# Kernel tuning notes

Measured on AMD Instinct MI355X. Metric: run time of the kernel, lower is better.

## Reference

```python
import jax, jax.numpy as jnp
import numpy as np

N_NODES = 50000
N_EDGES = 800000
D = 128


def setup_inputs() -> dict:
    key = jax.random.key(0)
    ks = jax.random.split(key, 8)
    s = 1.0 / np.sqrt(D)
    return {
        "x": jax.random.normal(ks[0], (N_NODES, D), dtype=jnp.float32),
        "edge_index": jax.random.randint(ks[1], (2, N_EDGES), 0, N_NODES, dtype=jnp.int32),
        "W0l": jax.random.normal(ks[2], (D, D), dtype=jnp.float32) * s,
        "b0l": jnp.zeros((D,), dtype=jnp.float32),
        "W0r": jax.random.normal(ks[3], (D, D), dtype=jnp.float32) * s,
        "W1l": jax.random.normal(ks[4], (D, D), dtype=jnp.float32) * s,
        "b1l": jnp.zeros((D,), dtype=jnp.float32),
        "W1r": jax.random.normal(ks[5], (D, D), dtype=jnp.float32) * s,
    }


def reference(x, edge_index, W0l, b0l, W0r, W1l, b1l, W1r):
    # Encoder(conv='sage', num_layers=2), eval mode (dropout = identity).
    src = edge_index[0]  # x_j gathered from source nodes
    dst = edge_index[1]  # aggregated at target nodes
    # in-degree for mean aggregation; isolated nodes get 0 aggregate (PyG mean)
    deg = jax.ops.segment_sum(jnp.ones_like(dst, dtype=x.dtype), dst, num_segments=N_NODES)
    inv_deg = jnp.where(deg > 0, 1.0 / jnp.maximum(deg, 1.0), 0.0)[:, None]

    def sage(h, Wl, bl, Wr):
        m = h @ Wl + bl                                        # lin_l
        agg = jax.ops.segment_sum(m[src], dst, num_segments=N_NODES) * inv_deg  # mean aggr
        return agg + h @ Wr                                    # + lin_r skip

    h = jax.nn.relu(sage(x, W0l, b0l, W0r))   # layer 0 + relu
    return sage(h, W1l, b1l, W1r)             # final layer
```

## Files before the change

kernel.cpp:

```cpp
#include <hip/hip_runtime.h>

#define N_NODES 50000
#define N_EDGES 800000
#define D 128
#define NBLK ((N_NODES + 255) / 256)
#define EPB 4096
#define CAP 8192

typedef __bf16 bf16x8 __attribute__((ext_vector_type(8)));
typedef short s16x8 __attribute__((ext_vector_type(8)));
typedef float f32x4 __attribute__((ext_vector_type(4)));
typedef unsigned short u16;
typedef unsigned int u32;
typedef u32 u32x2 __attribute__((ext_vector_type(2)));

__device__ inline u16 f32_to_bf16(float f) {
    u32 u = __builtin_bit_cast(u32, f);
    u += 0x7fffu + ((u >> 16) & 1u);
    return (u16)(u >> 16);
}
__device__ inline float bf16_lo(u32 v) { return __builtin_bit_cast(float, v << 16); }
__device__ inline float bf16_hi(u32 v) { return __builtin_bit_cast(float, v & 0xffff0000u); }

__device__ inline f32x4 mfma16(s16x8 a, s16x8 b, f32x4 c) {
    return __builtin_amdgcn_mfma_f32_16x16x32_bf16(
        __builtin_bit_cast(bf16x8, a), __builtin_bit_cast(bf16x8, b), c, 0, 0, 0);
}

#define CAST_BLOCKS ((N_NODES * 16) / 256)

__global__ __launch_bounds__(256) void prep_cast(
    const float* __restrict__ x, u16* __restrict__ xb,
    const float* __restrict__ W0l, const float* __restrict__ W0r,
    const float* __restrict__ W1l, const float* __restrict__ W1r,
    u16* __restrict__ Wp) {
    int b = blockIdx.x;
    if (b < CAST_BLOCKS) {
        int gid = b * 256 + threadIdx.x;
        const float* p = x + (size_t)gid * 8;
        f32x4 a = *(const f32x4*)p;
        f32x4 c = *(const f32x4*)(p + 4);
        u16 o[8];
#pragma unroll
        for (int j = 0; j < 4; j++) { o[j] = f32_to_bf16(a[j]); o[4 + j] = f32_to_bf16(c[j]); }
        *(s16x8*)(xb + (size_t)gid * 8) = *(const s16x8*)o;
    } else {
        int gid = (b - CAST_BLOCKS) * 256 + threadIdx.x;
        int wsel = gid >> 11;
        int rem  = gid & 2047;
        int ct   = rem >> 8;
        int ks   = (rem >> 6) & 3;
        int lane = rem & 63;
        const float* W = (wsel == 0) ? W0l : (wsel == 1) ? W0r : (wsel == 2) ? W1l : W1r;
        int n  = ct * 16 + (lane & 15);
        int k0 = ks * 32 + (lane >> 4) * 8;
        u16 o[8];
#pragma unroll
        for (int j = 0; j < 8; j++) o[j] = f32_to_bf16(W[(k0 + j) * D + n]);
        u16* dst = Wp + wsel * 16384 + (size_t)((ct * 4 + ks) * 64 + lane) * 8;
        *(s16x8*)dst = *(const s16x8*)o;
    }
}

__global__ __launch_bounds__(256) void stage_kernel(const int* __restrict__ src,
                                                    const int* __restrict__ dst,
                                                    int* __restrict__ ccount,
                                                    u32* __restrict__ staged) {
    __shared__ int hist[NBLK];
    __shared__ int base[NBLK];
    int t = threadIdx.x, b = blockIdx.x;
    int bb = b * EPB;
    if (t < NBLK) hist[t] = 0;
    __syncthreads();
    u32 pk[16]; int cb[16];
#pragma unroll
    for (int i = 0; i < 16; i++) {
        int e = bb + i * 256 + t;
        if (e < N_EDGES) {
            int sv = src[e], dv = dst[e];
            pk[i] = (u32)sv | ((u32)(dv & 255) << 16);
            cb[i] = dv >> 8;
            atomicAdd(&hist[cb[i]], 1);
        } else cb[i] = -1;
    }
    __syncthreads();
    if (t < NBLK) {
        int c = hist[t];
        if (c > 0) {
            int old = atomicAdd(&ccount[t], c);
            if (old > CAP - c) old = CAP - c;
            base[t] = t * CAP + old;
        }
        hist[t] = 0;
    }
    __syncthreads();
#pragma unroll
    for (int i = 0; i < 16; i++) {
        if (cb[i] >= 0) {
            int slot = atomicAdd(&hist[cb[i]], 1);
            staged[base[cb[i]] + slot] = pk[i];
        }
    }
}

__global__ __launch_bounds__(256) void fine_kernel(const int* __restrict__ ccount,
                                                   const u32* __restrict__ staged,
                                                   u16* __restrict__ eidx,
                                                   int* __restrict__ rowptr,
                                                   float* __restrict__ inv) {
    __shared__ u32 sdata[CAP];
    __shared__ int hist[256];
    __shared__ int cursor[256];
    __shared__ int sc[256];
    __shared__ int wsum[4];
    int t = threadIdx.x, cb = blockIdx.x;
    int lane = t & 63, wave = t >> 6;

    int cc = (t < NBLK) ? ccount[t] : 0;
    int cv = cc > CAP ? CAP : cc;
    int s = cv;
#pragma unroll
    for (int off = 1; off < 64; off <<= 1) {
        int u = __shfl_up(s, off, 64);
        if (lane >= off) s += u;
    }
    if (lane == 63) wsum[wave] = s;
    hist[t] = 0;
    __syncthreads();
    int wadd = 0;
#pragma unroll
    for (int w = 0; w < 4; w++) if (w < wave) wadd += wsum[w];
    sc[t] = s - cv + wadd;
    __syncthreads();
    int gbase = sc[cb];
    int c = ccount[cb];
    if (c > CAP) c = CAP;

    for (int i = t; i < c; i += 256) {
        u32 v = staged[cb * CAP + i];
        sdata[i] = v;
        atomicAdd(&hist[(v >> 16) & 255], 1);
    }
    __syncthreads();
    int d = hist[t];
    s = d;
#pragma unroll
    for (int off = 1; off < 64; off <<= 1) {
        int u = __shfl_up(s, off, 64);
        if (lane >= off) s += u;
    }
    if (lane == 63) wsum[wave] = s;
    __syncthreads();
    wadd = 0;
#pragma unroll
    for (int w = 0; w < 4; w++) if (w < wave) wadd += wsum[w];
    int excl = gbase + s - d + wadd;
    int node = cb * 256 + t;
    if (node < N_NODES) {
        rowptr[node] = excl;
        inv[node] = d > 0 ? 1.0f / (float)d : 0.0f;
    }
    cursor[t] = excl;
    if (cb == 0 && t == 0) rowptr[N_NODES] = N_EDGES;
    __syncthreads();
    for (int i = t; i < c; i += 256) {
        u32 v = sdata[i];
        int pos = atomicAdd(&cursor[(v >> 16) & 255], 1);
        eidx[pos] = (u16)(v & 0xffffu);
    }
}

__global__ __launch_bounds__(256) void agg_mean(const u16* __restrict__ h,
                                                const int* __restrict__ rowptr,
                                                const u16* __restrict__ eidx,
                                                const float* __restrict__ inv,
                                                u16* __restrict__ mean) {
    int wave = threadIdx.x >> 6, lane = threadIdx.x & 63;
    int node = blockIdx.x * 4 + wave;
    if (node >= N_NODES) return;
    int half = lane >> 5;
    int hl = lane & 31;
    int start = rowptr[node], end = rowptr[node + 1];

    float a0 = 0.f, a1 = 0.f, a2 = 0.f, a3 = 0.f;
    int e = start + half;
    for (; e + 6 < end; e += 8) {
        int s0 = eidx[e], s1 = eidx[e + 2], s2 = eidx[e + 4], s3 = eidx[e + 6];
        u32x2 v0 = *(const u32x2*)(h + (size_t)s0 * D + hl * 4);
        u32x2 v1 = *(const u32x2*)(h + (size_t)s1 * D + hl * 4);
        u32x2 v2 = *(const u32x2*)(h + (size_t)s2 * D + hl * 4);
        u32x2 v3 = *(const u32x2*)(h + (size_t)s3 * D + hl * 4);
        a0 += bf16_lo(v0.x) + bf16_lo(v1.x) + bf16_lo(v2.x) + bf16_lo(v3.x);
        a1 += bf16_hi(v0.x) + bf16_hi(v1.x) + bf16_hi(v2.x) + bf16_hi(v3.x);
        a2 += bf16_lo(v0.y) + bf16_lo(v1.y) + bf16_lo(v2.y) + bf16_lo(v3.y);
        a3 += bf16_hi(v0.y) + bf16_hi(v1.y) + bf16_hi(v2.y) + bf16_hi(v3.y);
    }
    for (; e < end; e += 2) {
        u32x2 v0 = *(const u32x2*)(h + (size_t)eidx[e] * D + hl * 4);
        a0 += bf16_lo(v0.x);
        a1 += bf16_hi(v0.x);
        a2 += bf16_lo(v0.y);
        a3 += bf16_hi(v0.y);
    }
    a0 += __shfl_xor(a0, 32);
    a1 += __shfl_xor(a1, 32);
    a2 += __shfl_xor(a2, 32);
    a3 += __shfl_xor(a3, 32);

    if (half == 0) {
        float iv = inv[node];
        u32x2 o;
        o.x = (u32)f32_to_bf16(a0 * iv) | ((u32)f32_to_bf16(a1 * iv) << 16);
        o.y = (u32)f32_to_bf16(a2 * iv) | ((u32)f32_to_bf16(a3 * iv) << 16);
        *(u32x2*)(mean + (size_t)node * D + hl * 4) = o;
    }
}

template <int RELU, int OUTF32>
__global__ __launch_bounds__(256) void gemm_fused(
    const u16* __restrict__ A1, const u16* __restrict__ A2,
    const u16* __restrict__ WpR, const u16* __restrict__ WpL,
    const float* __restrict__ bias, const float* __restrict__ inv,
    u16* __restrict__ outb, float* __restrict__ outf, int M) {
    int wave = threadIdx.x >> 6, lane = threadIdx.x & 63;
    int rowbase = blockIdx.x * 64;
    int lrow = lane & 15, quad = lane >> 4;

    s16x8 bR[2][4], bL[2][4];
#pragma unroll
    for (int ct = 0; ct < 2; ct++) {
        int ctg = wave * 2 + ct;
#pragma unroll
        for (int ks = 0; ks < 4; ks++) {
            size_t off = (size_t)((ctg * 4 + ks) * 64 + lane) * 8;
            bR[ct][ks] = *(const s16x8*)(WpR + off);
            bL[ct][ks] = *(const s16x8*)(WpL + off);
        }
    }

    f32x4 acc[4][2];
#pragma unroll
    for (int rt = 0; rt < 4; rt++)
#pragma unroll
        for (int ct = 0; ct < 2; ct++) acc[rt][ct] = (f32x4){0.f, 0.f, 0.f, 0.f};

#pragma unroll
    for (int ks = 0; ks < 4; ks++) {
        s16x8 a1[4], a2[4];
#pragma unroll
        for (int rt = 0; rt < 4; rt++) {
            int row = rowbase + rt * 16 + lrow;
            row = row < M ? row : M - 1;
            a1[rt] = *(const s16x8*)(A1 + (size_t)row * D + ks * 32 + quad * 8);
            a2[rt] = *(const s16x8*)(A2 + (size_t)row * D + ks * 32 + quad * 8);
        }
#pragma unroll
        for (int rt = 0; rt < 4; rt++)
#pragma unroll
            for (int ct = 0; ct < 2; ct++) {
                acc[rt][ct] = mfma16(a1[rt], bR[ct][ks], acc[rt][ct]);
                acc[rt][ct] = mfma16(a2[rt], bL[ct][ks], acc[rt][ct]);
            }
    }

    float bv[2];
#pragma unroll
    for (int ct = 0; ct < 2; ct++) bv[ct] = bias[wave * 32 + ct * 16 + lrow];

#pragma unroll
    for (int rt = 0; rt < 4; rt++) {
#pragma unroll
        for (int i = 0; i < 4; i++) {
            int row = rowbase + rt * 16 + quad * 4 + i;
            if (row >= M) continue;
            float mask = inv[row] > 0.f ? 1.f : 0.f;
#pragma unroll
            for (int ct = 0; ct < 2; ct++) {
                int col = wave * 32 + ct * 16 + lrow;
                float v = acc[rt][ct][i] + mask * bv[ct];
                if (RELU) v = v > 0.f ? v : 0.f;
                if (OUTF32) outf[(size_t)row * D + col] = v;
                else        outb[(size_t)row * D + col] = f32_to_bf16(v);
            }
        }
    }
}

extern "C" void kernel_launch(void* const* d_in, const int* in_sizes, int n_in,
                              void* d_out, int out_size, void* d_ws, size_t ws_size,
                              hipStream_t stream) {
    const float* x    = (const float*)d_in[0];
    const int*   edge = (const int*)d_in[1];
    const int*   src  = edge;
    const int*   dstn = edge + N_EDGES;
    const float* W0l  = (const float*)d_in[2];
    const float* b0l  = (const float*)d_in[3];
    const float* W0r  = (const float*)d_in[4];
    const float* W1l  = (const float*)d_in[5];
    const float* b1l  = (const float*)d_in[6];
    const float* W1r  = (const float*)d_in[7];
    float* out = (float*)d_out;

    char* p = (char*)d_ws;
    auto alloc = [&](size_t nb) { char* r = p; p += (nb + 255) & ~(size_t)255; return r; };
    int*   ccount = (int*)alloc((size_t)NBLK * 4);
    int*   rowptr = (int*)alloc((size_t)(N_NODES + 1) * 4);
    float* inv    = (float*)alloc((size_t)N_NODES * 4);
    u32*   staged = (u32*)alloc((size_t)NBLK * CAP * 4);
    u16*   eidx   = (u16*)alloc((size_t)N_EDGES * 2);
    u16*   xb     = (u16*)alloc((size_t)N_NODES * D * 2);
    u16*   hb     = (u16*)alloc((size_t)N_NODES * D * 2);
    u16*   meanb  = (u16*)alloc((size_t)N_NODES * D * 2);
    u16*   Wp     = (u16*)alloc((size_t)4 * 16384 * 2);

    hipMemsetAsync(ccount, 0, (size_t)NBLK * 4, stream);

    prep_cast<<<CAST_BLOCKS + 32, 256, 0, stream>>>(x, xb, W0l, W0r, W1l, W1r, Wp);
    stage_kernel<<<(N_EDGES + EPB - 1) / EPB, 256, 0, stream>>>(src, dstn, ccount, staged);
    fine_kernel<<<NBLK, 256, 0, stream>>>(ccount, staged, eidx, rowptr, inv);

    int mblocks = (N_NODES + 63) / 64;
    int ablocks = (N_NODES + 3) / 4;
    const u16* WpL0 = Wp;
    const u16* WpR0 = Wp + 16384;
    const u16* WpL1 = Wp + 2 * 16384;
    const u16* WpR1 = Wp + 3 * 16384;
    agg_mean<<<ablocks, 256, 0, stream>>>(xb, rowptr, eidx, inv, meanb);
    gemm_fused<1, 0><<<mblocks, 256, 0, stream>>>(xb, meanb, WpR0, WpL0, b0l, inv, hb, nullptr, N_NODES);
    agg_mean<<<ablocks, 256, 0, stream>>>(hb, rowptr, eidx, inv, meanb);
    gemm_fused<0, 1><<<mblocks, 256, 0, stream>>>(hb, meanb, WpR1, WpL1, b1l, inv, nullptr, out, N_NODES);
}
```

Before: 225.6 us.

## Merge cast and edge staging kernels; widen aggregation loads to 16 bytes

The x/weight bf16 cast and the edge bucketing stage now run as one kernel launch, with block ranges dispatching to each role. This removes a launch and lets the two independent phases overlap. The mean aggregation kernel now splits each wave into four groups of 16 lanes. Each lane loads 16 bytes (8 bf16) per neighbor row and accumulates 8 values, followed by a two-step shuffle reduction. This gives fewer, wider gather loads per edge, at the cost of more registers and more shuffles.

Measured after the change: 222.5 us. No clear change (-1.3%).

```diff
diff --git a/kernel.cpp b/kernel.cpp
--- a/kernel.cpp
+++ b/kernel.cpp
@@ -13,6 +13,7 @@
 typedef unsigned short u16;
 typedef unsigned int u32;
 typedef u32 u32x2 __attribute__((ext_vector_type(2)));
+typedef u32 u32x4 __attribute__((ext_vector_type(4)));
 
 __device__ inline u16 f32_to_bf16(float f) {
     u32 u = __builtin_bit_cast(u32, f);
@@ -28,15 +29,20 @@
 }
 
 #define CAST_BLOCKS ((N_NODES * 16) / 256)
-
-__global__ __launch_bounds__(256) void prep_cast(
+#define STAGE_BLOCKS ((N_EDGES + EPB - 1) / EPB)
+
+__global__ __launch_bounds__(256) void prep_stage(
     const float* __restrict__ x, u16* __restrict__ xb,
     const float* __restrict__ W0l, const float* __restrict__ W0r,
     const float* __restrict__ W1l, const float* __restrict__ W1r,
-    u16* __restrict__ Wp) {
-    int b = blockIdx.x;
+    u16* __restrict__ Wp,
+    const int* __restrict__ src, const int* __restrict__ dst,
+    int* __restrict__ ccount, u32* __restrict__ staged) {
+    __shared__ int hist[NBLK];
+    __shared__ int base[NBLK];
+    int t = threadIdx.x, b = blockIdx.x;
     if (b < CAST_BLOCKS) {
-        int gid = b * 256 + threadIdx.x;
+        int gid = b * 256 + t;
         const float* p = x + (size_t)gid * 8;
         f32x4 a = *(const f32x4*)p;
         f32x4 c = *(const f32x4*)(p + 4);
@@ -44,8 +50,8 @@
 #pragma unroll
         for (int j = 0; j < 4; j++) { o[j] = f32_to_bf16(a[j]); o[4 + j] = f32_to_bf16(c[j]); }
         *(s16x8*)(xb + (size_t)gid * 8) = *(const s16x8*)o;
-    } else {
-        int gid = (b - CAST_BLOCKS) * 256 + threadIdx.x;
+    } else if (b < CAST_BLOCKS + 32) {
+        int gid = (b - CAST_BLOCKS) * 256 + t;
         int wsel = gid >> 11;
         int rem  = gid & 2047;
         int ct   = rem >> 8;
@@ -57,48 +63,41 @@
         u16 o[8];
 #pragma unroll
         for (int j = 0; j < 8; j++) o[j] = f32_to_bf16(W[(k0 + j) * D + n]);
-        u16* dst = Wp + wsel * 16384 + (size_t)((ct * 4 + ks) * 64 + lane) * 8;
-        *(s16x8*)dst = *(const s16x8*)o;
-    }
-}
-
-__global__ __launch_bounds__(256) void stage_kernel(const int* __restrict__ src,
-                                                    const int* __restrict__ dst,
-                                                    int* __restrict__ ccount,
-                                                    u32* __restrict__ staged) {
-    __shared__ int hist[NBLK];
-    __shared__ int base[NBLK];
-    int t = threadIdx.x, b = blockIdx.x;
-    int bb = b * EPB;
-    if (t < NBLK) hist[t] = 0;
-    __syncthreads();
-    u32 pk[16]; int cb[16];
-#pragma unroll
-    for (int i = 0; i < 16; i++) {
-        int e = bb + i * 256 + t;
-        if (e < N_EDGES) {
-            int sv = src[e], dv = dst[e];
-            pk[i] = (u32)sv | ((u32)(dv & 255) << 16);
-            cb[i] = dv >> 8;
-            atomicAdd(&hist[cb[i]], 1);
-        } else cb[i] = -1;
-    }
-    __syncthreads();
-    if (t < NBLK) {
-        int c = hist[t];
-        if (c > 0) {
-            int old = atomicAdd(&ccount[t], c);
-            if (old > CAP - c) old = CAP - c;
-            base[t] = t * CAP + old;
-        }
-        hist[t] = 0;
-    }
-    __syncthreads();
-#pragma unroll
-    for (int i = 0; i < 16; i++) {
-        if (cb[i] >= 0) {
-            int slot = atomicAdd(&hist[cb[i]], 1);
-            staged[base[cb[i]] + slot] = pk[i];
+        u16* dp = Wp + wsel * 16384 + (size_t)((ct * 4 + ks) * 64 + lane) * 8;
+        *(s16x8*)dp = *(const s16x8*)o;
+    } else {
+        int sb = b - CAST_BLOCKS - 32;
+        int bb = sb * EPB;
+        if (t < NBLK) hist[t] = 0;
+        __syncthreads();
+        u32 pk[16]; int cb[16];
+#pragma unroll
+        for (int i = 0; i < 16; i++) {
+            int e = bb + i * 256 + t;
+            if (e < N_EDGES) {
+                int sv = src[e], dv = dst[e];
+                pk[i] = (u32)sv | ((u32)(dv & 255) << 16);
+                cb[i] = dv >> 8;
+                atomicAdd(&hist[cb[i]], 1);
+            } else cb[i] = -1;
+        }
+        __syncthreads();
+        if (t < NBLK) {
+            int c = hist[t];
+            if (c > 0) {
+                int old = atomicAdd(&ccount[t], c);
+                if (old > CAP - c) old = CAP - c;
+                base[t] = t * CAP + old;
+            }
+            hist[t] = 0;
+        }
+        __syncthreads();
+#pragma unroll
+        for (int i = 0; i < 16; i++) {
+            if (cb[i] >= 0) {
+                int slot = atomicAdd(&hist[cb[i]], 1);
+                staged[base[cb[i]] + slot] = pk[i];
+            }
         }
     }
 }
@@ -178,41 +177,55 @@
     int wave = threadIdx.x >> 6, lane = threadIdx.x & 63;
     int node = blockIdx.x * 4 + wave;
     if (node >= N_NODES) return;
-    int half = lane >> 5;
-    int hl = lane & 31;
+    int quad = lane >> 4;
+    int ql = lane & 15;
     int start = rowptr[node], end = rowptr[node + 1];
 
-    float a0 = 0.f, a1 = 0.f, a2 = 0.f, a3 = 0.f;
-    int e = start + half;
-    for (; e + 6 < end; e += 8) {
-        int s0 = eidx[e], s1 = eidx[e + 2], s2 = eidx[e + 4], s3 = eidx[e + 6];
-        u32x2 v0 = *(const u32x2*)(h + (size_t)s0 * D + hl * 4);
-        u32x2 v1 = *(const u32x2*)(h + (size_t)s1 * D + hl * 4);
-        u32x2 v2 = *(const u32x2*)(h + (size_t)s2 * D + hl * 4);
-        u32x2 v3 = *(const u32x2*)(h + (size_t)s3 * D + hl * 4);
+    float a0=0.f,a1=0.f,a2=0.f,a3=0.f,a4=0.f,a5=0.f,a6=0.f,a7=0.f;
+    int base = start;
+    for (; base + 16 <= end; base += 16) {
+        int i0 = base + quad;
+        int s0 = eidx[i0], s1 = eidx[i0 + 4], s2 = eidx[i0 + 8], s3 = eidx[i0 + 12];
+        u32x4 v0 = *(const u32x4*)(h + (size_t)s0 * D + ql * 8);
+        u32x4 v1 = *(const u32x4*)(h + (size_t)s1 * D + ql * 8);
+        u32x4 v2 = *(const u32x4*)(h + (size_t)s2 * D + ql * 8);
+        u32x4 v3 = *(const u32x4*)(h + (size_t)s3 * D + ql * 8);
         a0 += bf16_lo(v0.x) + bf16_lo(v1.x) + bf16_lo(v2.x) + bf16_lo(v3.x);
         a1 += bf16_hi(v0.x) + bf16_hi(v1.x) + bf16_hi(v2.x) + bf16_hi(v3.x);
         a2 += bf16_lo(v0.y) + bf16_lo(v1.y) + bf16_lo(v2.y) + bf16_lo(v3.y);
         a3 += bf16_hi(v0.y) + bf16_hi(v1.y) + bf16_hi(v2.y) + bf16_hi(v3.y);
-    }
-    for (; e < end; e += 2) {
-        u32x2 v0 = *(const u32x2*)(h + (size_t)eidx[e] * D + hl * 4);
-        a0 += bf16_lo(v0.x);
-        a1 += bf16_hi(v0.x);
-        a2 += bf16_lo(v0.y);
-        a3 += bf16_hi(v0.y);
-    }
-    a0 += __shfl_xor(a0, 32);
-    a1 += __shfl_xor(a1, 32);
-    a2 += __shfl_xor(a2, 32);
-    a3 += __shfl_xor(a3, 32);
-
-    if (half == 0) {
+        a4 += bf16_lo(v0.z) + bf16_lo(v1.z) + bf16_lo(v2.z) + bf16_lo(v3.z);
+        a5 += bf16_hi(v0.z) + bf16_hi(v1.z) + bf16_hi(v2.z) + bf16_hi(v3.z);
+        a6 += bf16_lo(v0.w) + bf16_lo(v1.w) + bf16_lo(v2.w) + bf16_lo(v3.w);
+        a7 += bf16_hi(v0.w) + bf16_hi(v1.w) + bf16_hi(v2.w) + bf16_hi(v3.w);
+    }
+    for (; base < end; base += 4) {
+        int i = base + quad;
+        if (i < end) {
+            u32x4 v = *(const u32x4*)(h + (size_t)eidx[i] * D + ql * 8);
+            a0 += bf16_lo(v.x); a1 += bf16_hi(v.x);
+            a2 += bf16_lo(v.y); a3 += bf16_hi(v.y);
+            a4 += bf16_lo(v.z); a5 += bf16_hi(v.z);
+            a6 += bf16_lo(v.w); a7 += bf16_hi(v.w);
+        }
+    }
+    a0 += __shfl_xor(a0, 16); a0 += __shfl_xor(a0, 32);
+    a1 += __shfl_xor(a1, 16); a1 += __shfl_xor(a1, 32);
+    a2 += __shfl_xor(a2, 16); a2 += __shfl_xor(a2, 32);
+    a3 += __shfl_xor(a3, 16); a3 += __shfl_xor(a3, 32);
+    a4 += __shfl_xor(a4, 16); a4 += __shfl_xor(a4, 32);
+    a5 += __shfl_xor(a5, 16); a5 += __shfl_xor(a5, 32);
+    a6 += __shfl_xor(a6, 16); a6 += __shfl_xor(a6, 32);
+    a7 += __shfl_xor(a7, 16); a7 += __shfl_xor(a7, 32);
+
+    if (quad == 0) {
         float iv = inv[node];
-        u32x2 o;
+        u32x4 o;
         o.x = (u32)f32_to_bf16(a0 * iv) | ((u32)f32_to_bf16(a1 * iv) << 16);
         o.y = (u32)f32_to_bf16(a2 * iv) | ((u32)f32_to_bf16(a3 * iv) << 16);
-        *(u32x2*)(mean + (size_t)node * D + hl * 4) = o;
+        o.z = (u32)f32_to_bf16(a4 * iv) | ((u32)f32_to_bf16(a5 * iv) << 16);
+        o.w = (u32)f32_to_bf16(a6 * iv) | ((u32)f32_to_bf16(a7 * iv) << 16);
+        *(u32x4*)(mean + (size_t)node * D + ql * 8) = o;
     }
 }
 
@@ -315,8 +328,8 @@
 
     hipMemsetAsync(ccount, 0, (size_t)NBLK * 4, stream);
 
-    prep_cast<<<CAST_BLOCKS + 32, 256, 0, stream>>>(x, xb, W0l, W0r, W1l, W1r, Wp);
-    stage_kernel<<<(N_EDGES + EPB - 1) / EPB, 256, 0, stream>>>(src, dstn, ccount, staged);
+    prep_stage<<<CAST_BLOCKS + 32 + STAGE_BLOCKS, 256, 0, stream>>>(
+        x, xb, W0l, W0r, W1l, W1r, Wp, src, dstn, ccount, staged);
     fine_kernel<<<NBLK, 256, 0, stream>>>(ccount, staged, eidx, rowptr, inv);
 
     int mblocks = (N_NODES + 63) / 64;
```
